# Kernel tuning notes

Measured on AMD Instinct MI355X. Metric: run time of the kernel, lower is better.

Reference implementation:

```python
import jax, jax.numpy as jnp
import numpy as np

KERNEL_SIZE = 3
DILATION = 1


def setup_inputs() -> dict:
    key = jax.random.key(0)
    k1, k2, k3 = jax.random.split(key, 3)
    B, C, T = 8, 512, 4096
    OUT = 512
    x = jax.random.normal(k1, (B, C, T), dtype=jnp.float32)
    # nn.Linear weight: (out_features, in_features=C*kernel_size)
    W = jax.random.normal(k2, (OUT, C * KERNEL_SIZE), dtype=jnp.float32) * 0.02
    b = jax.random.normal(k3, (OUT,), dtype=jnp.float32) * 0.02
    return {"x": x, "W": W, "b": b}


def reference(x, W, b):
    # UnfoldConv1d forward: causal unfold (im2col) -> transpose -> linear -> transpose.
    # TemporalUnfold1d left-pads with (k-1)*dilation zeros, unfolds with kernel k,
    # then gathers rows so the feature axis is ordered (kernel_pos, channel):
    # row j*C + c at time t equals x[b, c, t - (k-1-j)*dilation] (zero-padded).
    K, D = KERNEL_SIZE, DILATION
    B, C, T = x.shape
    pad = (K - 1) * D
    xp = jnp.pad(x, ((0, 0), (0, 0), (pad, 0)))  # (B, C, T+pad)
    # unf[b, j, c, t] = xp[b, c, t + j*D] ; j=K-1 corresponds to current timestep
    unf = jnp.stack([xp[:, :, j * D: j * D + T] for j in range(K)], axis=1)  # (B, K, C, T)
    unf = unf.reshape(B, K * C, T)
    # transpose(1,2) -> linear -> transpose(1,2) == einsum over feature axis
    y = jnp.einsum('bft,of->bot', unf, W) + b[None, :, None]  # (B, OUT, T)
    return y
```

## Files before the change

### kernel.cpp

```cpp
#include <hip/hip_runtime.h>
#include <stdint.h>


typedef float    f32x4  __attribute__((ext_vector_type(4)));
typedef short    bf16x8 __attribute__((ext_vector_type(8)));

#define C_DIM   512
#define T_DIM   4096
#define TP_DIM  4104
#define OUT_DIM 512
#define KF_DIM  1536
#define B_DIM   8

__device__ __forceinline__ uint16_t f2bf(float f) {
  union { float f; uint32_t u; } v; v.f = f;
  uint32_t u = v.u;
  return (uint16_t)((u + 0x7fffu + ((u >> 16) & 1u)) >> 16);
}

__device__ __forceinline__ void gload_lds16(const uint16_t* g, uint16_t* l) {
  __builtin_amdgcn_global_load_lds(
      (const __attribute__((address_space(1))) uint32_t*)g,
      (__attribute__((address_space(3))) uint32_t*)l, 16, 0, 0);
}

__device__ __forceinline__ void stage_slab(const uint16_t* __restrict__ srcbase,
                                           int stride, uint16_t* lds, int r0,
                                           int tid) {
  int row = r0 + (tid >> 3);
  int ch = tid & 7;
  const uint16_t* src = srcbase + (long)row * stride + ((ch ^ (row & 7)) << 3);
  gload_lds16(src, lds + (((r0 << 3) + ((tid >> 6) << 6)) << 3));
}

#define PH_MID() do { __builtin_amdgcn_s_barrier(); \
  asm volatile("s_waitcnt lgkmcnt(0)" ::: "memory"); \
  __builtin_amdgcn_sched_barrier(0); \
  __builtin_amdgcn_s_setprio(1); } while (0)

#define PH_END() do { __builtin_amdgcn_s_setprio(0); \
  __builtin_amdgcn_s_barrier(); } while (0)

#define READ_A(BUF, MH) do { \
  _Pragma("unroll") for (int mi = 0; mi < 4; ++mi) { \
    int row = wm * 128 + (MH) * 64 + mi * 16 + lr; \
    _Pragma("unroll") for (int kk = 0; kk < 2; ++kk) \
      af[mi][kk] = *(const bf16x8*)&(BUF)[row * 64 + (((kk * 4 + g) ^ (row & 7)) << 3)]; \
  } } while (0)

#define READ_B(BUF, NH) do { \
  _Pragma("unroll") for (int ni = 0; ni < 2; ++ni) { \
    int row = wn * 64 + (NH) * 32 + ni * 16 + lr; \
    _Pragma("unroll") for (int kk = 0; kk < 2; ++kk) \
      bfr[NH][ni][kk] = *(const bf16x8*)&(BUF)[row * 64 + (((kk * 4 + g) ^ (row & 7)) << 3)]; \
  } } while (0)

#define QUAD(MH, NH) do { \
  _Pragma("unroll") for (int mi = 0; mi < 4; ++mi) \
  _Pragma("unroll") for (int ni = 0; ni < 2; ++ni) \
  _Pragma("unroll") for (int kk = 0; kk < 2; ++kk) \
    acc[(MH) * 4 + mi][(NH) * 2 + ni] = __builtin_amdgcn_mfma_f32_16x16x32_bf16( \
        af[mi][kk], bfr[NH][ni][kk], acc[(MH) * 4 + mi][(NH) * 2 + ni], 0, 0, 0); \
  } while (0)

template<bool FULL>
__device__ __forceinline__ void iter8(
    f32x4 (&acc)[8][4],
    uint16_t* LA0, uint16_t* LB0, uint16_t* LA1, uint16_t* LB1,
    const uint16_t* __restrict__ wsrc,
    const uint16_t* __restrict__ xsrc,
    int kb0, int tid, int wm, int wn, int lr, int g) {
  const uint16_t* a1 = wsrc + (kb0 + 1) * 64;
  const uint16_t* a2 = wsrc + (kb0 + 2) * 64;
  const uint16_t* a3 = wsrc + (kb0 + 3) * 64;
  const uint16_t* b2 = xsrc + ((kb0 + 2) >> 3) * C_DIM + (((kb0 + 2) & 7) << 6);
  const uint16_t* b3 = xsrc + ((kb0 + 3) >> 3) * C_DIM + (((kb0 + 3) & 7) << 6);

  bf16x8 af[4][2];
  bf16x8 bfr[2][2][2];

  READ_A(LA0, 0); READ_B(LB0, 0);
  stage_slab(a1, KF_DIM, LA1, 64, tid); stage_slab(a1, KF_DIM, LA1, 192, tid);
  PH_MID(); QUAD(0, 0); PH_END();
  READ_B(LB0, 1);
  if (FULL) { stage_slab(a2, KF_DIM, LA0, 0, tid); stage_slab(a2, KF_DIM, LA0, 128, tid); }
  PH_MID(); QUAD(0, 1); PH_END();
  READ_A(LA0, 1);
  if (FULL) { stage_slab(b2, C_DIM, LB0, 0, tid); stage_slab(b2, C_DIM, LB0, 64, tid); }
  PH_MID(); QUAD(1, 1); PH_END();
  if (FULL) { stage_slab(b2, C_DIM, LB0, 128, tid); stage_slab(b2, C_DIM, LB0, 192, tid); }
  PH_MID(); QUAD(1, 0);
  __builtin_amdgcn_s_setprio(0);
  if (FULL) asm volatile("s_waitcnt vmcnt(6)" ::: "memory");
  else      asm volatile("s_waitcnt vmcnt(0)" ::: "memory");
  __builtin_amdgcn_s_barrier();
  READ_A(LA1, 0); READ_B(LB1, 0);
  if (FULL) { stage_slab(a2, KF_DIM, LA0, 64, tid); stage_slab(a2, KF_DIM, LA0, 192, tid); }
  PH_MID(); QUAD(0, 0); PH_END();
  READ_B(LB1, 1);
  if (FULL) { stage_slab(a3, KF_DIM, LA1, 0, tid); stage_slab(a3, KF_DIM, LA1, 128, tid); }
  PH_MID(); QUAD(0, 1); PH_END();
  READ_A(LA1, 1);
  if (FULL) { stage_slab(b3, C_DIM, LB1, 0, tid); stage_slab(b3, C_DIM, LB1, 64, tid); }
  PH_MID(); QUAD(1, 1); PH_END();
  if (FULL) { stage_slab(b3, C_DIM, LB1, 128, tid); stage_slab(b3, C_DIM, LB1, 192, tid); }
  PH_MID(); QUAD(1, 0);
  __builtin_amdgcn_s_setprio(0);
  if (FULL) asm volatile("s_waitcnt vmcnt(6)" ::: "memory");
  __builtin_amdgcn_s_barrier();
}

__global__ __launch_bounds__(512, 2) void gemm_kernel(
    const uint16_t* __restrict__ xp, const uint16_t* __restrict__ Wb,
    const float* __restrict__ bias, float* __restrict__ out) {
  __shared__ __align__(16) uint16_t LA0[256 * 64];
  __shared__ __align__(16) uint16_t LB0[256 * 64];
  __shared__ __align__(16) uint16_t LA1[256 * 64];
  __shared__ __align__(16) uint16_t LB1[256 * 64];

  const int tid  = threadIdx.x;
  const int lane = tid & 63;
  const int wid  = tid >> 6;
  const int wm   = wid >> 2;
  const int wn   = wid & 3;
  const int lr   = lane & 15;
  const int g    = lane >> 4;
  const int t0 = blockIdx.x * 256;
  const int o0 = blockIdx.y * 256;
  const int b  = blockIdx.z;

  const uint16_t* wsrc = Wb + (long)o0 * KF_DIM;
  const uint16_t* xsrc = xp + ((long)b * TP_DIM + t0) * C_DIM;

  f32x4 acc[8][4];
  #pragma unroll
  for (int mi = 0; mi < 8; ++mi)
    #pragma unroll
    for (int ni = 0; ni < 4; ++ni)
      #pragma unroll
      for (int r = 0; r < 4; ++r) acc[mi][ni][r] = 0.0f;

  const uint16_t* a0 = wsrc;
  const uint16_t* a1 = wsrc + 64;
  const uint16_t* b0 = xsrc;
  const uint16_t* b1 = xsrc + 64;
  stage_slab(a0, KF_DIM, LA0, 0, tid);   stage_slab(a0, KF_DIM, LA0, 64, tid);
  stage_slab(a0, KF_DIM, LA0, 128, tid); stage_slab(a0, KF_DIM, LA0, 192, tid);
  stage_slab(b0, C_DIM, LB0, 0, tid);    stage_slab(b0, C_DIM, LB0, 64, tid);
  stage_slab(b0, C_DIM, LB0, 128, tid);  stage_slab(b0, C_DIM, LB0, 192, tid);
  stage_slab(a1, KF_DIM, LA1, 0, tid);   stage_slab(a1, KF_DIM, LA1, 128, tid);
  stage_slab(b1, C_DIM, LB1, 0, tid);    stage_slab(b1, C_DIM, LB1, 64, tid);
  stage_slab(b1, C_DIM, LB1, 128, tid);  stage_slab(b1, C_DIM, LB1, 192, tid);
  asm volatile("s_waitcnt vmcnt(6)" ::: "memory");
  __builtin_amdgcn_s_barrier();

  #pragma unroll 1
  for (int i = 0; i < 11; ++i)
    iter8<true>(acc, LA0, LB0, LA1, LB1, wsrc, xsrc, 2 * i, tid, wm, wn, lr, g);
  iter8<false>(acc, LA0, LB0, LA1, LB1, wsrc, xsrc, 22, tid, wm, wn, lr, g);

  #pragma unroll
  for (int mi = 0; mi < 8; ++mi) {
    int orow = o0 + wm * 128 + mi * 16 + (lane >> 4) * 4;
    #pragma unroll
    for (int ni = 0; ni < 4; ++ni) {
      int t = t0 + wn * 64 + ni * 16 + lr;
      float* op = out + ((long)b * OUT_DIM + orow) * T_DIM + t;
      #pragma unroll
      for (int r = 0; r < 4; ++r)
        op[(long)r * T_DIM] = acc[mi][ni][r] + bias[orow + r];
    }
  }
}

__global__ __launch_bounds__(256) void prep_w(const float* __restrict__ W,
                                              uint16_t* __restrict__ Wb) {
  int i = blockIdx.x * 256 + threadIdx.x;
  if (i >= 196608) return;
  float4 v = ((const float4*)W)[i];
  ushort4 o;
  o.x = f2bf(v.x); o.y = f2bf(v.y); o.z = f2bf(v.z); o.w = f2bf(v.w);
  ((ushort4*)Wb)[i] = o;
}

__global__ __launch_bounds__(256) void prep_x(const float* __restrict__ x,
                                              uint16_t* __restrict__ xp) {
  __shared__ uint16_t tile[64 * 66];
  const int tid = threadIdx.x;
  const int tp0 = blockIdx.x * 64;
  const int c0  = blockIdx.y * 64;
  const int b   = blockIdx.z;
  #pragma unroll
  for (int it = 0; it < 8; ++it) {
    int u = it * 256 + tid;
    int crow = u >> 5;
    int p = u & 31;
    int t = tp0 - 2 + p * 2;
    float vx = 0.f, vy = 0.f;
    if (t >= 0 && t < T_DIM) {
      const float2 v = *(const float2*)(x + (long)(b * C_DIM + c0 + crow) * T_DIM + t);
      vx = v.x; vy = v.y;
    }
    tile[(2 * p) * 66 + crow]     = f2bf(vx);
    tile[(2 * p + 1) * 66 + crow] = f2bf(vy);
  }
  __syncthreads();
  #pragma unroll
  for (int it = 0; it < 8; ++it) {
    int u = it * 256 + tid;
    int tl = u >> 5;
    int q = u & 31;
    int tp = tp0 + tl;
    if (tp < TP_DIM) {
      ushort2 val;
      val.x = tile[tl * 66 + 2 * q];
      val.y = tile[tl * 66 + 2 * q + 1];
      *(ushort2*)(xp + (long)(b * TP_DIM + tp) * C_DIM + c0 + 2 * q) = val;
    }
  }
}

__global__ __launch_bounds__(256) void naive_kernel(const float* __restrict__ x,
                                                    const float* __restrict__ W,
                                                    const float* __restrict__ bias,
                                                    float* __restrict__ y) {
  int t = blockIdx.x * 256 + threadIdx.x;
  int o = blockIdx.y, b = blockIdx.z;
  float s = bias[o];
  #pragma unroll
  for (int j = 0; j < 3; ++j) {
    int tt = t - 2 + j;
    if (tt < 0) continue;
    const float* xr = x + (long)b * C_DIM * T_DIM + tt;
    const float* wr = W + (long)o * KF_DIM + j * C_DIM;
    float a = 0.f;
    for (int c = 0; c < C_DIM; ++c) a += wr[c] * xr[(long)c * T_DIM];
    s += a;
  }
  y[((long)b * OUT_DIM + o) * T_DIM + t] = s;
}

extern "C" void kernel_launch(void* const* d_in, const int* in_sizes, int n_in,
                              void* d_out, int out_size, void* d_ws, size_t ws_size,
                              hipStream_t stream) {
  (void)in_sizes; (void)n_in; (void)out_size;
  const float* x    = (const float*)d_in[0];
  const float* W    = (const float*)d_in[1];
  const float* bias = (const float*)d_in[2];
  float* out = (float*)d_out;

  const size_t wb_elems = (size_t)OUT_DIM * KF_DIM;
  const size_t xp_elems = (size_t)B_DIM * TP_DIM * C_DIM;
  const size_t need = (wb_elems + xp_elems) * sizeof(uint16_t);

  if (ws_size < need) {
    naive_kernel<<<dim3(T_DIM / 256, OUT_DIM, B_DIM), 256, 0, stream>>>(x, W, bias, out);
    return;
  }

  uint16_t* Wb = (uint16_t*)d_ws;
  uint16_t* xp = (uint16_t*)d_ws + wb_elems;

  prep_w<<<768, 256, 0, stream>>>(W, Wb);
  prep_x<<<dim3(65, 8, 8), 256, 0, stream>>>(x, xp);
  gemm_kernel<<<dim3(16, 2, 8), 512, 0, stream>>>(xp, Wb, bias, out);
}
```

Baseline: 90.37 us.

## Restructure GEMM main loop into 8-phase ping-pong with register-carried fragments

```diff
diff --git a/kernel.cpp b/kernel.cpp
--- a/kernel.cpp
+++ b/kernel.cpp
@@ -30,84 +30,105 @@
   int row = r0 + (tid >> 3);
   int ch = tid & 7;
   const uint16_t* src = srcbase + (long)row * stride + ((ch ^ (row & 7)) << 3);
-  gload_lds16(src, lds + (((r0 << 3) + ((tid >> 6) << 6)) << 3));
-}
-
-#define PH_MID() do { __builtin_amdgcn_s_barrier(); \
-  asm volatile("s_waitcnt lgkmcnt(0)" ::: "memory"); \
-  __builtin_amdgcn_sched_barrier(0); \
-  __builtin_amdgcn_s_setprio(1); } while (0)
-
-#define PH_END() do { __builtin_amdgcn_s_setprio(0); \
-  __builtin_amdgcn_s_barrier(); } while (0)
-
-#define READ_A(BUF, MH) do { \
+  gload_lds16(src, lds + (long)(r0 * 64 + (tid >> 6) * 512));
+}
+
+#define BAR()   __builtin_amdgcn_s_barrier()
+#define SBAR()  __builtin_amdgcn_sched_barrier(0)
+#define LGKM(n) do { asm volatile("s_waitcnt lgkmcnt(" #n ")" ::: "memory"); SBAR(); } while (0)
+#define VM(n)   asm volatile("s_waitcnt vmcnt(" #n ")" ::: "memory")
+#define PRIO1() __builtin_amdgcn_s_setprio(1)
+#define PRIO0() __builtin_amdgcn_s_setprio(0)
+
+#define READ_A(dst, BUF, MH) do { \
   _Pragma("unroll") for (int mi = 0; mi < 4; ++mi) { \
-    int row = wm * 128 + (MH) * 64 + mi * 16 + lr; \
+    const int row_ = wm * 128 + (MH) * 64 + mi * 16 + lr; \
     _Pragma("unroll") for (int kk = 0; kk < 2; ++kk) \
-      af[mi][kk] = *(const bf16x8*)&(BUF)[row * 64 + (((kk * 4 + g) ^ (row & 7)) << 3)]; \
+      dst[mi][kk] = *(const bf16x8*)&(BUF)[row_ * 64 + (((kk * 4 + g) ^ (row_ & 7)) << 3)]; \
   } } while (0)
 
-#define READ_B(BUF, NH) do { \
+#define READ_B(dst, BUF, NH) do { \
   _Pragma("unroll") for (int ni = 0; ni < 2; ++ni) { \
-    int row = wn * 64 + (NH) * 32 + ni * 16 + lr; \
+    const int row_ = wn * 64 + (NH) * 32 + ni * 16 + lr; \
     _Pragma("unroll") for (int kk = 0; kk < 2; ++kk) \
-      bfr[NH][ni][kk] = *(const bf16x8*)&(BUF)[row * 64 + (((kk * 4 + g) ^ (row & 7)) << 3)]; \
+      dst[ni][kk] = *(const bf16x8*)&(BUF)[row_ * 64 + (((kk * 4 + g) ^ (row_ & 7)) << 3)]; \
   } } while (0)
 
-#define QUAD(MH, NH) do { \
+#define QUAD(A, B, MH, NH) do { PRIO1(); \
   _Pragma("unroll") for (int mi = 0; mi < 4; ++mi) \
   _Pragma("unroll") for (int ni = 0; ni < 2; ++ni) \
   _Pragma("unroll") for (int kk = 0; kk < 2; ++kk) \
     acc[(MH) * 4 + mi][(NH) * 2 + ni] = __builtin_amdgcn_mfma_f32_16x16x32_bf16( \
-        af[mi][kk], bfr[NH][ni][kk], acc[(MH) * 4 + mi][(NH) * 2 + ni], 0, 0, 0); \
-  } while (0)
+        A[mi][kk], B[ni][kk], acc[(MH) * 4 + mi][(NH) * 2 + ni], 0, 0, 0); \
+  PRIO0(); } while (0)
 
 template<bool FULL>
 __device__ __forceinline__ void iter8(
     f32x4 (&acc)[8][4],
+    bf16x8 (&a0)[4][2], bf16x8 (&a1)[4][2],
+    bf16x8 (&b0)[2][2], bf16x8 (&b1)[2][2],
     uint16_t* LA0, uint16_t* LB0, uint16_t* LA1, uint16_t* LB1,
-    const uint16_t* __restrict__ wsrc,
-    const uint16_t* __restrict__ xsrc,
+    const uint16_t* __restrict__ wsrc, const uint16_t* __restrict__ xsrc,
     int kb0, int tid, int wm, int wn, int lr, int g) {
-  const uint16_t* a1 = wsrc + (kb0 + 1) * 64;
-  const uint16_t* a2 = wsrc + (kb0 + 2) * 64;
-  const uint16_t* a3 = wsrc + (kb0 + 3) * 64;
-  const uint16_t* b2 = xsrc + ((kb0 + 2) >> 3) * C_DIM + (((kb0 + 2) & 7) << 6);
-  const uint16_t* b3 = xsrc + ((kb0 + 3) >> 3) * C_DIM + (((kb0 + 3) & 7) << 6);
-
-  bf16x8 af[4][2];
-  bf16x8 bfr[2][2][2];
-
-  READ_A(LA0, 0); READ_B(LB0, 0);
-  stage_slab(a1, KF_DIM, LA1, 64, tid); stage_slab(a1, KF_DIM, LA1, 192, tid);
-  PH_MID(); QUAD(0, 0); PH_END();
-  READ_B(LB0, 1);
-  if (FULL) { stage_slab(a2, KF_DIM, LA0, 0, tid); stage_slab(a2, KF_DIM, LA0, 128, tid); }
-  PH_MID(); QUAD(0, 1); PH_END();
-  READ_A(LA0, 1);
-  if (FULL) { stage_slab(b2, C_DIM, LB0, 0, tid); stage_slab(b2, C_DIM, LB0, 64, tid); }
-  PH_MID(); QUAD(1, 1); PH_END();
-  if (FULL) { stage_slab(b2, C_DIM, LB0, 128, tid); stage_slab(b2, C_DIM, LB0, 192, tid); }
-  PH_MID(); QUAD(1, 0);
-  __builtin_amdgcn_s_setprio(0);
-  if (FULL) asm volatile("s_waitcnt vmcnt(6)" ::: "memory");
-  else      asm volatile("s_waitcnt vmcnt(0)" ::: "memory");
-  __builtin_amdgcn_s_barrier();
-  READ_A(LA1, 0); READ_B(LB1, 0);
-  if (FULL) { stage_slab(a2, KF_DIM, LA0, 64, tid); stage_slab(a2, KF_DIM, LA0, 192, tid); }
-  PH_MID(); QUAD(0, 0); PH_END();
-  READ_B(LB1, 1);
-  if (FULL) { stage_slab(a3, KF_DIM, LA1, 0, tid); stage_slab(a3, KF_DIM, LA1, 128, tid); }
-  PH_MID(); QUAD(0, 1); PH_END();
-  READ_A(LA1, 1);
-  if (FULL) { stage_slab(b3, C_DIM, LB1, 0, tid); stage_slab(b3, C_DIM, LB1, 64, tid); }
-  PH_MID(); QUAD(1, 1); PH_END();
-  if (FULL) { stage_slab(b3, C_DIM, LB1, 128, tid); stage_slab(b3, C_DIM, LB1, 192, tid); }
-  PH_MID(); QUAD(1, 0);
-  __builtin_amdgcn_s_setprio(0);
-  if (FULL) asm volatile("s_waitcnt vmcnt(6)" ::: "memory");
-  __builtin_amdgcn_s_barrier();
+  const uint16_t* bO1 = xsrc + ((kb0 + 1) >> 3) * C_DIM + (((kb0 + 1) & 7) << 6);
+  const uint16_t* aE = wsrc + (kb0 + 2) * 64;
+  const uint16_t* aO = wsrc + (kb0 + 3) * 64;
+  const uint16_t* bE = xsrc + ((kb0 + 2) >> 3) * C_DIM + (((kb0 + 2) & 7) << 6);
+  const uint16_t* bO = xsrc + ((kb0 + 3) >> 3) * C_DIM + (((kb0 + 3) & 7) << 6);
+
+  BAR();
+  READ_B(b1, LB0, 1);
+  stage_slab(bO1, C_DIM, LB1, 128, tid); stage_slab(bO1, C_DIM, LB1, 192, tid);
+  LGKM(4);
+  QUAD(a0, b0, 0, 0);
+  VM(8);
+  BAR();
+  READ_A(a1, LA0, 1);
+  if (FULL) { stage_slab(aE, KF_DIM, LA0, 0, tid); stage_slab(aE, KF_DIM, LA0, 128, tid); }
+  LGKM(8);
+  QUAD(a0, b1, 0, 1);
+  if (FULL) VM(8); else VM(6);
+  BAR();
+  READ_A(a0, LA1, 0);
+  if (FULL) { stage_slab(bE, C_DIM, LB0, 0, tid); stage_slab(bE, C_DIM, LB0, 64, tid); }
+  LGKM(8);
+  QUAD(a1, b1, 1, 1);
+  if (FULL) VM(4); else VM(0);
+  BAR();
+  READ_B(b1, LB1, 1);
+  if (FULL) { stage_slab(bE, C_DIM, LB0, 128, tid); stage_slab(bE, C_DIM, LB0, 192, tid); }
+  LGKM(4);
+  QUAD(a1, b0, 1, 0);
+  BAR();
+  READ_B(b0, LB1, 0);
+  if (FULL) { stage_slab(aE, KF_DIM, LA0, 64, tid); stage_slab(aE, KF_DIM, LA0, 192, tid); }
+  LGKM(4);
+  QUAD(a0, b1, 0, 1);
+  BAR();
+  READ_A(a1, LA1, 1);
+  if (FULL) { stage_slab(aO, KF_DIM, LA1, 0, tid); stage_slab(aO, KF_DIM, LA1, 128, tid); }
+  LGKM(8);
+  QUAD(a0, b0, 0, 0);
+  if (FULL) VM(8);
+  BAR();
+  if (FULL) {
+    READ_A(a0, LA0, 0);
+    stage_slab(bO, C_DIM, LB1, 0, tid); stage_slab(bO, C_DIM, LB1, 64, tid);
+    LGKM(8);
+  } else {
+    LGKM(0);
+  }
+  QUAD(a1, b0, 1, 0);
+  if (FULL) VM(6);
+  BAR();
+  if (FULL) {
+    READ_B(b0, LB0, 0);
+    stage_slab(aO, KF_DIM, LA1, 64, tid); stage_slab(aO, KF_DIM, LA1, 192, tid);
+    LGKM(4);
+  } else {
+    LGKM(0);
+  }
+  QUAD(a1, b1, 1, 1);
 }
 
 __global__ __launch_bounds__(512, 2) void gemm_kernel(
@@ -140,24 +161,30 @@
       #pragma unroll
       for (int r = 0; r < 4; ++r) acc[mi][ni][r] = 0.0f;
 
-  const uint16_t* a0 = wsrc;
-  const uint16_t* a1 = wsrc + 64;
-  const uint16_t* b0 = xsrc;
-  const uint16_t* b1 = xsrc + 64;
-  stage_slab(a0, KF_DIM, LA0, 0, tid);   stage_slab(a0, KF_DIM, LA0, 64, tid);
-  stage_slab(a0, KF_DIM, LA0, 128, tid); stage_slab(a0, KF_DIM, LA0, 192, tid);
-  stage_slab(b0, C_DIM, LB0, 0, tid);    stage_slab(b0, C_DIM, LB0, 64, tid);
-  stage_slab(b0, C_DIM, LB0, 128, tid);  stage_slab(b0, C_DIM, LB0, 192, tid);
-  stage_slab(a1, KF_DIM, LA1, 0, tid);   stage_slab(a1, KF_DIM, LA1, 128, tid);
-  stage_slab(b1, C_DIM, LB1, 0, tid);    stage_slab(b1, C_DIM, LB1, 64, tid);
-  stage_slab(b1, C_DIM, LB1, 128, tid);  stage_slab(b1, C_DIM, LB1, 192, tid);
-  asm volatile("s_waitcnt vmcnt(6)" ::: "memory");
-  __builtin_amdgcn_s_barrier();
+  bf16x8 a0[4][2], a1[4][2], b0r[2][2], b1r[2][2];
+
+  stage_slab(wsrc, KF_DIM, LA0, 0, tid);   stage_slab(wsrc, KF_DIM, LA0, 128, tid);
+  stage_slab(xsrc, C_DIM, LB0, 0, tid);    stage_slab(xsrc, C_DIM, LB0, 64, tid);
+  stage_slab(xsrc, C_DIM, LB0, 128, tid);  stage_slab(xsrc, C_DIM, LB0, 192, tid);
+  VM(0);
+  BAR();
+  READ_A(a0, LA0, 0);
+  READ_B(b0r, LB0, 0);
+  stage_slab(wsrc, KF_DIM, LA0, 64, tid);  stage_slab(wsrc, KF_DIM, LA0, 192, tid);
+  {
+    const uint16_t* a1p = wsrc + 64;
+    const uint16_t* b1p = xsrc + 64;
+    stage_slab(a1p, KF_DIM, LA1, 0, tid);  stage_slab(a1p, KF_DIM, LA1, 128, tid);
+    stage_slab(b1p, C_DIM, LB1, 0, tid);   stage_slab(b1p, C_DIM, LB1, 64, tid);
+    stage_slab(a1p, KF_DIM, LA1, 64, tid); stage_slab(a1p, KF_DIM, LA1, 192, tid);
+  }
 
   #pragma unroll 1
   for (int i = 0; i < 11; ++i)
-    iter8<true>(acc, LA0, LB0, LA1, LB1, wsrc, xsrc, 2 * i, tid, wm, wn, lr, g);
-  iter8<false>(acc, LA0, LB0, LA1, LB1, wsrc, xsrc, 22, tid, wm, wn, lr, g);
+    iter8<true>(acc, a0, a1, b0r, b1r, LA0, LB0, LA1, LB1, wsrc, xsrc,
+                2 * i, tid, wm, wn, lr, g);
+  iter8<false>(acc, a0, a1, b0r, b1r, LA0, LB0, LA1, LB1, wsrc, xsrc,
+               22, tid, wm, wn, lr, g);
 
   #pragma unroll
   for (int mi = 0; mi < 8; ++mi) {
```

Result: slower. 137.0 us (+51.6%).
